# Kernel optimization log

Measured on AMD Instinct MI355X. Metric: run time of the kernel, lower is better.

The kernel has to match this reference:

```python
import jax, jax.numpy as jnp
import numpy as np

B, S, D = 4, 4096, 64
NEG = 1e31  # matches the torch module's -1e+31 masking constant


def setup_inputs() -> dict:
    key = jax.random.key(0)
    kq, kk, kv = jax.random.split(key, 3)
    return {
        "query": jax.random.normal(kq, (B, S, D), dtype=jnp.float32),
        "key": jax.random.normal(kk, (B, S, D), dtype=jnp.float32),
        "value": jax.random.normal(kv, (B, S, D), dtype=jnp.float32),
    }


def reference(query, key, value):
    # scores: [B, Sq, Sk]
    attn_weights = jnp.einsum("bqd,bkd->bqk", query, key)
    # NOTE: original subtracts the causal penalty BEFORE the sqrt(d) scaling
    Sq, Sk = query.shape[1], key.shape[1]
    causal_mask = jnp.triu(jnp.ones((Sq, Sk), dtype=attn_weights.dtype), k=1)
    attn_weights = attn_weights - causal_mask[None, :, :] * NEG
    attn_weights = attn_weights / np.sqrt(key.shape[-1]).astype(np.float32)
    attn_weights = jax.nn.softmax(attn_weights, axis=-1)
    # dropout p=0.0 -> identity on value
    attn_vec = jnp.einsum("bqk,bkd->bqd", attn_weights, value)
    return attn_vec, attn_weights
```

## Files before the change

### kernel.cpp

```cpp
#include <hip/hip_runtime.h>

#define SQ 4096
#define DD 64
#define NB 4
#define NEL (NB*SQ*DD)

typedef __attribute__((ext_vector_type(4))) float f32x4;
typedef __attribute__((ext_vector_type(8))) __bf16 bf16x8;

__device__ __forceinline__ unsigned short f2bf(float f) {
  unsigned int u = __builtin_bit_cast(unsigned int, f);
  u = (u + 0x7FFFu + ((u >> 16) & 1u)) >> 16;
  return (unsigned short)u;
}

__device__ __forceinline__ bf16x8 ldfrag(const unsigned short* p) {
  uint4 u = *(const uint4*)p;
  return __builtin_bit_cast(bf16x8, u);
}

__device__ __forceinline__ bf16x8 pack_bf8(f32x4 a, f32x4 b) {
  bf16x8 r;
  r[0] = (__bf16)a[0]; r[1] = (__bf16)a[1]; r[2] = (__bf16)a[2]; r[3] = (__bf16)a[3];
  r[4] = (__bf16)b[0]; r[5] = (__bf16)b[1]; r[6] = (__bf16)b[2]; r[7] = (__bf16)b[3];
  return r;
}

__global__ __launch_bounds__(256) void prep_kernel(
    const float* __restrict__ q, const float* __restrict__ k,
    const float* __restrict__ v, unsigned short* __restrict__ ws)
{
  unsigned short* qbf = ws;
  unsigned short* kbf = ws + (size_t)NEL;
  unsigned short* vt  = ws + 2*(size_t)NEL;
  const int bid = blockIdx.x;
  const int tid = threadIdx.x;
  if (bid < 1024) {
    const float* src = (bid < 512) ? q : k;
    unsigned short* dst = (bid < 512) ? qbf : kbf;
    const int base = (bid & 511) * 512 + tid;
#pragma unroll
    for (int i = 0; i < 2; ++i) {
      int idx = base + i * 256;
      float4 f = ((const float4*)src)[idx];
      ushort4 o;
      o.x = f2bf(f.x); o.y = f2bf(f.y); o.z = f2bf(f.z); o.w = f2bf(f.w);
      ((ushort4*)dst)[idx] = o;
    }
  } else {
    __shared__ unsigned short tile[64][66];
    const int t  = bid - 1024;
    const int bb = t >> 6;
    const int st = t & 63;
    const float* vb = v + (size_t)bb * SQ * DD + (size_t)st * 64 * DD;
    const int r  = tid >> 4;
    const int c4 = tid & 15;
#pragma unroll
    for (int j = 0; j < 4; ++j) {
      int row = r + j * 16;
      float4 f = ((const float4*)(vb + (size_t)row * DD))[c4];
      tile[row][c4 * 4 + 0] = f2bf(f.x);
      tile[row][c4 * 4 + 1] = f2bf(f.y);
      tile[row][c4 * 4 + 2] = f2bf(f.z);
      tile[row][c4 * 4 + 3] = f2bf(f.w);
    }
    __syncthreads();
    unsigned short* vtb = vt + (size_t)bb * DD * SQ;
#pragma unroll
    for (int j = 0; j < 4; ++j) {
      int d   = r + j * 16;
      int s0l = c4 * 4;
      ushort4 o;
      o.x = tile[s0l + 0][d];
      o.y = tile[s0l + 1][d];
      o.z = tile[s0l + 2][d];
      o.w = tile[s0l + 3][d];
      ((ushort4*)(vtb + (size_t)d * SQ + st * 64))[c4] = o;
    }
  }
}

__global__ __launch_bounds__(512, 6) void lsum_kernel(
    const unsigned short* __restrict__ qbf,
    const unsigned short* __restrict__ kbf,
    float* __restrict__ li2_g)
{
  __shared__ float lred[8][4][4];
  const int tid  = threadIdx.x;
  const int wave = tid >> 6;
  const int lane = tid & 63;
  const int l16  = lane & 15;
  const int quad = lane >> 4;

  const int bidx = blockIdx.x;
  const int b    = bidx & 3;
  const int qt   = 255 - (bidx >> 2);

  const unsigned short* Qb = qbf + (size_t)b * SQ * DD;
  const unsigned short* Kb = kbf + (size_t)b * SQ * DD;
  const int q0    = qt * 16;
  const int rowg0 = q0 + quad * 4;

  bf16x8 aQ0, aQ1;
  {
    const unsigned short* qrow = Qb + (size_t)(q0 + l16) * DD + quad * 8;
    aQ0 = ldfrag(qrow);
    aQ1 = ldfrag(qrow + 32);
  }

  const int nkt = (qt >> 2) + 1;
  const float SC = 0.125f * 1.4426950408889634f;
  const f32x4 zf = {0.f, 0.f, 0.f, 0.f};

  float lsum[4] = {0.f, 0.f, 0.f, 0.f};
  for (int kt = wave; kt < nkt; kt += 8) {
    const int k0 = kt * 64;
    f32x4 acc[4] = {zf, zf, zf, zf};
#pragma unroll
    for (int ct = 0; ct < 4; ++ct) {
      const unsigned short* krow = Kb + (size_t)(k0 + ct * 16 + l16) * DD + quad * 8;
      bf16x8 b0 = ldfrag(krow);
      bf16x8 b1 = ldfrag(krow + 32);
      acc[ct] = __builtin_amdgcn_mfma_f32_16x16x32_bf16(aQ0, b0, acc[ct], 0, 0, 0);
      acc[ct] = __builtin_amdgcn_mfma_f32_16x16x32_bf16(aQ1, b1, acc[ct], 0, 0, 0);
    }
#pragma unroll
    for (int ct = 0; ct < 4; ++ct) {
      const int colg = k0 + ct * 16 + l16;
#pragma unroll
      for (int r = 0; r < 4; ++r) {
        float tt = (colg <= rowg0 + r) ? acc[ct][r] * SC : -1e30f;
        lsum[r] += __builtin_amdgcn_exp2f(tt);
      }
    }
  }
#pragma unroll
  for (int r = 0; r < 4; ++r) {
    float v = lsum[r];
    v += __shfl_xor(v, 1);
    v += __shfl_xor(v, 2);
    v += __shfl_xor(v, 4);
    v += __shfl_xor(v, 8);
    lsum[r] = v;
  }
  if (l16 == 0) {
#pragma unroll
    for (int r = 0; r < 4; ++r) lred[wave][quad][r] = lsum[r];
  }
  __syncthreads();
  if (tid < 16) {
    float s = 0.f;
#pragma unroll
    for (int w = 0; w < 8; ++w) s += lred[w][tid >> 2][tid & 3];
    li2_g[(size_t)b * SQ + q0 + tid] = -__builtin_amdgcn_logf(s);
  }
}

__global__ __launch_bounds__(512, 4) void wo_kernel(
    const unsigned short* __restrict__ qbf,
    const unsigned short* __restrict__ kbf,
    const unsigned short* __restrict__ vtp,
    const float* __restrict__ li2_g,
    float* __restrict__ out_vec,
    float* __restrict__ out_w)
{
  __shared__ __align__(16) float pt[8][16][132];

  const int tid  = threadIdx.x;
  const int wave = tid >> 6;
  const int lane = tid & 63;
  const int l16  = lane & 15;
  const int quad = lane >> 4;
  const int half = lane >> 5;
  const int c32  = lane & 31;

  const int bidx = blockIdx.x;
  const int b    = bidx & 3;
  const int qt   = 255 - (bidx >> 2);

  const unsigned short* Qb = qbf + (size_t)b * SQ * DD;
  const unsigned short* Kb = kbf + (size_t)b * SQ * DD;
  const unsigned short* Vt = vtp + (size_t)b * DD * SQ;
  float* Wb = out_w  + (size_t)b * SQ * SQ;
  float* Ob = out_vec + (size_t)b * SQ * DD;

  const int q0    = qt * 16;
  const int rowg0 = q0 + quad * 4;

  bf16x8 aQ0, aQ1;
  {
    const unsigned short* qrow = Qb + (size_t)(q0 + l16) * DD + quad * 8;
    aQ0 = ldfrag(qrow);
    aQ1 = ldfrag(qrow + 32);
  }

  float li2[4];
#pragma unroll
  for (int r = 0; r < 4; ++r)
    li2[r] = li2_g[(size_t)b * SQ + rowg0 + r];

  const int nkt = (qt >> 2) + 1;
  const int nst = (nkt + 1) >> 1;
  const float SC = 0.125f * 1.4426950408889634f;
  const f32x4 zf = {0.f, 0.f, 0.f, 0.f};
  f32x4 accO[4] = {zf, zf, zf, zf};

  for (int st = wave; st < nst; st += 8) {
    const int k0c = st * 128;
#pragma unroll
    for (int h = 0; h < 2; ++h) {
      const int k0 = k0c + h * 64;
      f32x4 acc[4] = {zf, zf, zf, zf};
#pragma unroll
      for (int ct = 0; ct < 4; ++ct) {
        const unsigned short* krow = Kb + (size_t)(k0 + ct * 16 + l16) * DD + quad * 8;
        bf16x8 b0 = ldfrag(krow);
        bf16x8 b1 = ldfrag(krow + 32);
        acc[ct] = __builtin_amdgcn_mfma_f32_16x16x32_bf16(aQ0, b0, acc[ct], 0, 0, 0);
        acc[ct] = __builtin_amdgcn_mfma_f32_16x16x32_bf16(aQ1, b1, acc[ct], 0, 0, 0);
      }
#pragma unroll
      for (int ct = 0; ct < 4; ++ct) {
        const int colg = k0 + ct * 16 + l16;
#pragma unroll
        for (int r = 0; r < 4; ++r) {
          float tt = (colg <= rowg0 + r) ? __builtin_fmaf(acc[ct][r], SC, li2[r])
                                         : -1e30f;
          pt[wave][quad * 4 + r][h * 64 + ct * 16 + l16] = __builtin_amdgcn_exp2f(tt);
        }
      }
    }
#pragma unroll
    for (int i = 0; i < 8; ++i) {
      const int rr = 2 * i + half;
      f32x4 pv = *(const f32x4*)&pt[wave][rr][c32 * 4];
      *(f32x4*)(Wb + (size_t)(q0 + rr) * SQ + k0c + c32 * 4) = pv;
    }
#pragma unroll
    for (int kk = 0; kk < 4; ++kk) {
      const float* pr = &pt[wave][l16][kk * 32 + quad * 8];
      f32x4 p0 = *(const f32x4*)pr;
      f32x4 p1 = *(const f32x4*)(pr + 4);
      bf16x8 aP = pack_bf8(p0, p1);
#pragma unroll
      for (int ct = 0; ct < 4; ++ct) {
        const unsigned short* vrow =
            Vt + (size_t)(ct * 16 + l16) * SQ + k0c + kk * 32 + quad * 8;
        bf16x8 bv = ldfrag(vrow);
        accO[ct] = __builtin_amdgcn_mfma_f32_16x16x32_bf16(aP, bv, accO[ct], 0, 0, 0);
      }
    }
  }

  float* ow_mine = &pt[wave][0][0];
#pragma unroll
  for (int ct = 0; ct < 4; ++ct)
#pragma unroll
    for (int r = 0; r < 4; ++r)
      ow_mine[(quad * 4 + r) * 64 + ct * 16 + l16] = accO[ct][r];
  __syncthreads();
#pragma unroll
  for (int i = 0; i < 2; ++i) {
    int idx = tid + i * 512;
    int row = idx >> 6, col = idx & 63;
    float s = 0.f;
#pragma unroll
    for (int w = 0; w < 8; ++w) s += pt[w][0][row * 64 + col];
    Ob[(size_t)(q0 + row) * DD + col] = s;
  }

  const int zc0 = nst * 128;
  const int nz4 = (SQ - zc0) >> 2;
  if (nz4 > 0) {
    const f32x4 z = {0.f, 0.f, 0.f, 0.f};
    for (int r = 0; r < 16; ++r) {
      f32x4* zp = (f32x4*)(Wb + (size_t)(q0 + r) * SQ + zc0);
      for (int i = tid; i < nz4; i += 512)
        zp[i] = z;
    }
  }
}

extern "C" void kernel_launch(void* const* d_in, const int* in_sizes, int n_in,
                              void* d_out, int out_size, void* d_ws, size_t ws_size,
                              hipStream_t stream) {
  const float* q = (const float*)d_in[0];
  const float* k = (const float*)d_in[1];
  const float* v = (const float*)d_in[2];
  float* out_vec = (float*)d_out;
  float* out_w   = out_vec + (size_t)NB * SQ * DD;
  unsigned short* ws = (unsigned short*)d_ws;
  float* li2_g = (float*)(ws + 3 * (size_t)NEL);

  hipLaunchKernelGGL(prep_kernel, dim3(1280), dim3(256), 0, stream, q, k, v, ws);
  hipLaunchKernelGGL(lsum_kernel, dim3(1024), dim3(512), 0, stream,
                     ws, ws + (size_t)NEL, li2_g);
  hipLaunchKernelGGL(wo_kernel, dim3(1024), dim3(512), 0, stream,
                     ws, ws + (size_t)NEL, ws + 2 * (size_t)NEL,
                     li2_g, out_vec, out_w);
}
```

Before: 353.1 us.

## Stage 1024-column P strips in shared LDS for coalesced full-row weight stores

Each block now processes 1024-column super-strips in which every wave computes a 128-column slice into one shared LDS tile, then block-synchronises. Each wave writes two complete 1024-wide rows of the attention-weight matrix, so global stores become long contiguous row segments instead of 128-column fragments per wave. Slices above the diagonal are zero-filled in LDS rather than computed. This adds two __syncthreads per strip and can leave waves idle on partially live strips, which costs load balance in exchange for better write coalescing on the large weight output.

```diff
diff --git a/kernel.cpp b/kernel.cpp
--- a/kernel.cpp
+++ b/kernel.cpp
@@ -1,4 +1,5 @@
 #include <hip/hip_runtime.h>
+
 
 #define SQ 4096
 #define DD 64
@@ -164,15 +165,13 @@
     float* __restrict__ out_vec,
     float* __restrict__ out_w)
 {
-  __shared__ __align__(16) float pt[8][16][132];
+  __shared__ __align__(16) float ptS[16][1044];
 
   const int tid  = threadIdx.x;
-  const int wave = tid >> 6;
+  const int wv   = tid >> 6;
   const int lane = tid & 63;
   const int l16  = lane & 15;
   const int quad = lane >> 4;
-  const int half = lane >> 5;
-  const int c32  = lane & 31;
 
   const int bidx = blockIdx.x;
   const int b    = bidx & 3;
@@ -199,60 +198,88 @@
   for (int r = 0; r < 4; ++r)
     li2[r] = li2_g[(size_t)b * SQ + rowg0 + r];
 
-  const int nkt = (qt >> 2) + 1;
-  const int nst = (nkt + 1) >> 1;
+  const int nkt  = (qt >> 2) + 1;
+  const int ncov = nkt * 64;
+  const int nstb = (nkt + 15) >> 4;
   const float SC = 0.125f * 1.4426950408889634f;
   const f32x4 zf = {0.f, 0.f, 0.f, 0.f};
   f32x4 accO[4] = {zf, zf, zf, zf};
 
-  for (int st = wave; st < nst; st += 8) {
-    const int k0c = st * 128;
-#pragma unroll
-    for (int h = 0; h < 2; ++h) {
-      const int k0 = k0c + h * 64;
-      f32x4 acc[4] = {zf, zf, zf, zf};
-#pragma unroll
-      for (int ct = 0; ct < 4; ++ct) {
-        const unsigned short* krow = Kb + (size_t)(k0 + ct * 16 + l16) * DD + quad * 8;
-        bf16x8 b0 = ldfrag(krow);
-        bf16x8 b1 = ldfrag(krow + 32);
-        acc[ct] = __builtin_amdgcn_mfma_f32_16x16x32_bf16(aQ0, b0, acc[ct], 0, 0, 0);
-        acc[ct] = __builtin_amdgcn_mfma_f32_16x16x32_bf16(aQ1, b1, acc[ct], 0, 0, 0);
-      }
-#pragma unroll
-      for (int ct = 0; ct < 4; ++ct) {
-        const int colg = k0 + ct * 16 + l16;
-#pragma unroll
-        for (int r = 0; r < 4; ++r) {
-          float tt = (colg <= rowg0 + r) ? __builtin_fmaf(acc[ct][r], SC, li2[r])
-                                         : -1e30f;
-          pt[wave][quad * 4 + r][h * 64 + ct * 16 + l16] = __builtin_amdgcn_exp2f(tt);
+  const int wc0 = wv * 128;
+
+  for (int s = 0; s < nstb; ++s) {
+    const int k0s  = s << 10;
+    const int c0   = k0s + wc0;
+    const bool live = (c0 <= q0 + 15);
+
+    if (live) {
+#pragma unroll
+      for (int h = 0; h < 2; ++h) {
+        const int k0 = c0 + h * 64;
+        f32x4 acc[4] = {zf, zf, zf, zf};
+#pragma unroll
+        for (int ct = 0; ct < 4; ++ct) {
+          const unsigned short* krow = Kb + (size_t)(k0 + ct * 16 + l16) * DD + quad * 8;
+          bf16x8 b0 = ldfrag(krow);
+          bf16x8 b1 = ldfrag(krow + 32);
+          acc[ct] = __builtin_amdgcn_mfma_f32_16x16x32_bf16(aQ0, b0, acc[ct], 0, 0, 0);
+          acc[ct] = __builtin_amdgcn_mfma_f32_16x16x32_bf16(aQ1, b1, acc[ct], 0, 0, 0);
         }
-      }
-    }
-#pragma unroll
-    for (int i = 0; i < 8; ++i) {
-      const int rr = 2 * i + half;
-      f32x4 pv = *(const f32x4*)&pt[wave][rr][c32 * 4];
-      *(f32x4*)(Wb + (size_t)(q0 + rr) * SQ + k0c + c32 * 4) = pv;
-    }
-#pragma unroll
-    for (int kk = 0; kk < 4; ++kk) {
-      const float* pr = &pt[wave][l16][kk * 32 + quad * 8];
-      f32x4 p0 = *(const f32x4*)pr;
-      f32x4 p1 = *(const f32x4*)(pr + 4);
-      bf16x8 aP = pack_bf8(p0, p1);
-#pragma unroll
-      for (int ct = 0; ct < 4; ++ct) {
-        const unsigned short* vrow =
-            Vt + (size_t)(ct * 16 + l16) * SQ + k0c + kk * 32 + quad * 8;
-        bf16x8 bv = ldfrag(vrow);
-        accO[ct] = __builtin_amdgcn_mfma_f32_16x16x32_bf16(aP, bv, accO[ct], 0, 0, 0);
-      }
-    }
-  }
-
-  float* ow_mine = &pt[wave][0][0];
+#pragma unroll
+        for (int ct = 0; ct < 4; ++ct) {
+          const int colg = k0 + ct * 16 + l16;
+#pragma unroll
+          for (int r = 0; r < 4; ++r) {
+            float tt = (colg <= rowg0 + r) ? __builtin_fmaf(acc[ct][r], SC, li2[r])
+                                           : -1e30f;
+            ptS[quad * 4 + r][wc0 + h * 64 + ct * 16 + l16] =
+                __builtin_amdgcn_exp2f(tt);
+          }
+        }
+      }
+    } else {
+#pragma unroll
+      for (int i = 0; i < 8; ++i) {
+        int idx = i * 64 + lane;
+        int row = idx >> 5;
+        int c4  = idx & 31;
+        *(f32x4*)&ptS[row][wc0 + c4 * 4] = zf;
+      }
+    }
+    __syncthreads();
+
+#pragma unroll
+    for (int rr = 0; rr < 2; ++rr) {
+      const int row = 2 * wv + rr;
+      float* wrow = Wb + (size_t)(q0 + row) * SQ + k0s;
+#pragma unroll
+      for (int i = 0; i < 4; ++i) {
+        f32x4 pv = *(const f32x4*)&ptS[row][i * 256 + lane * 4];
+        *(f32x4*)(wrow + i * 256 + lane * 4) = pv;
+      }
+    }
+
+    if (live) {
+#pragma unroll
+      for (int kk = 0; kk < 4; ++kk) {
+        const float* pr = &ptS[l16][wc0 + kk * 32 + quad * 8];
+        f32x4 p0 = *(const f32x4*)pr;
+        f32x4 p1 = *(const f32x4*)(pr + 4);
+        bf16x8 aP = pack_bf8(p0, p1);
+#pragma unroll
+        for (int ct = 0; ct < 4; ++ct) {
+          const unsigned short* vrow =
+              Vt + (size_t)(ct * 16 + l16) * SQ + c0 + kk * 32 + quad * 8;
+          bf16x8 bv = ldfrag(vrow);
+          accO[ct] = __builtin_amdgcn_mfma_f32_16x16x32_bf16(aP, bv, accO[ct], 0, 0, 0);
+        }
+      }
+    }
+    __syncthreads();
+  }
+
+  float* base = &ptS[0][0];
+  float* ow_mine = base + wv * 2088;
 #pragma unroll
   for (int ct = 0; ct < 4; ++ct)
 #pragma unroll
@@ -265,18 +292,17 @@
     int row = idx >> 6, col = idx & 63;
     float s = 0.f;
 #pragma unroll
-    for (int w = 0; w < 8; ++w) s += pt[w][0][row * 64 + col];
+    for (int w = 0; w < 8; ++w) s += base[w * 2088 + row * 64 + col];
     Ob[(size_t)(q0 + row) * DD + col] = s;
   }
 
-  const int zc0 = nst * 128;
+  const int zc0 = nstb << 10;
   const int nz4 = (SQ - zc0) >> 2;
   if (nz4 > 0) {
-    const f32x4 z = {0.f, 0.f, 0.f, 0.f};
     for (int r = 0; r < 16; ++r) {
       f32x4* zp = (f32x4*)(Wb + (size_t)(q0 + r) * SQ + zc0);
       for (int i = tid; i < nz4; i += 512)
-        zp[i] = z;
+        zp[i] = zf;
     }
   }
 }
```

Result: no change. 348.4 us (-1.3%).

## Fuse row-sum and output passes into one kernel with LDS-resident probabilities

Applied to the files above, without the earlier changes.

Merges the separate softmax-denominator kernel and the weights/output kernel into one attention kernel. The unnormalized exp scores are computed once, stored as bf16 in a full-row LDS buffer (16 rows × 4104), and then normalized while being written out and fed to the PV MFMA. This drops the second QK^T recompute and a kernel launch. In exchange it uses about 131KB of LDS per block, which lowers occupancy to 2 blocks per CU. The stored weights are also now rounded to bf16 before normalization, which may cost accuracy.

```diff
diff --git a/kernel.cpp b/kernel.cpp
--- a/kernel.cpp
+++ b/kernel.cpp
@@ -1,9 +1,11 @@
 #include <hip/hip_runtime.h>
+
 
 #define SQ 4096
 #define DD 64
 #define NB 4
 #define NEL (NB*SQ*DD)
+#define PSTRIDE 4104
 
 typedef __attribute__((ext_vector_type(4))) float f32x4;
 typedef __attribute__((ext_vector_type(8))) __bf16 bf16x8;
@@ -19,11 +21,8 @@
   return __builtin_bit_cast(bf16x8, u);
 }
 
-__device__ __forceinline__ bf16x8 pack_bf8(f32x4 a, f32x4 b) {
-  bf16x8 r;
-  r[0] = (__bf16)a[0]; r[1] = (__bf16)a[1]; r[2] = (__bf16)a[2]; r[3] = (__bf16)a[3];
-  r[4] = (__bf16)b[0]; r[5] = (__bf16)b[1]; r[6] = (__bf16)b[2]; r[7] = (__bf16)b[3];
-  return r;
+__device__ __forceinline__ float bf2f(unsigned short u) {
+  return __builtin_bit_cast(float, (unsigned int)u << 16);
 }
 
 __global__ __launch_bounds__(256) void prep_kernel(
@@ -80,12 +79,17 @@
   }
 }
 
-__global__ __launch_bounds__(512, 6) void lsum_kernel(
+__global__ __launch_bounds__(512, 2) void attn_kernel(
     const unsigned short* __restrict__ qbf,
     const unsigned short* __restrict__ kbf,
-    float* __restrict__ li2_g)
+    const unsigned short* __restrict__ vtp,
+    float* __restrict__ out_vec,
+    float* __restrict__ out_w)
 {
+  __shared__ __align__(16) unsigned short Ps[16 * PSTRIDE];
   __shared__ float lred[8][4][4];
+  __shared__ float inv_l_s[16];
+
   const int tid  = threadIdx.x;
   const int wave = tid >> 6;
   const int lane = tid & 63;
@@ -98,6 +102,10 @@
 
   const unsigned short* Qb = qbf + (size_t)b * SQ * DD;
   const unsigned short* Kb = kbf + (size_t)b * SQ * DD;
+  const unsigned short* Vt = vtp + (size_t)b * DD * SQ;
+  float* Wb = out_w  + (size_t)b * SQ * SQ;
+  float* Ob = out_vec + (size_t)b * SQ * DD;
+
   const int q0    = qt * 16;
   const int rowg0 = q0 + quad * 4;
 
@@ -108,32 +116,52 @@
     aQ1 = ldfrag(qrow + 32);
   }
 
-  const int nkt = (qt >> 2) + 1;
+  const int nkt  = (qt >> 2) + 1;
+  const int nch  = (nkt + 15) >> 4;
+  const int nstp = nch << 3;
   const float SC = 0.125f * 1.4426950408889634f;
   const f32x4 zf = {0.f, 0.f, 0.f, 0.f};
 
   float lsum[4] = {0.f, 0.f, 0.f, 0.f};
-  for (int kt = wave; kt < nkt; kt += 8) {
-    const int k0 = kt * 64;
-    f32x4 acc[4] = {zf, zf, zf, zf};
-#pragma unroll
-    for (int ct = 0; ct < 4; ++ct) {
-      const unsigned short* krow = Kb + (size_t)(k0 + ct * 16 + l16) * DD + quad * 8;
-      bf16x8 b0 = ldfrag(krow);
-      bf16x8 b1 = ldfrag(krow + 32);
-      acc[ct] = __builtin_amdgcn_mfma_f32_16x16x32_bf16(aQ0, b0, acc[ct], 0, 0, 0);
-      acc[ct] = __builtin_amdgcn_mfma_f32_16x16x32_bf16(aQ1, b1, acc[ct], 0, 0, 0);
-    }
-#pragma unroll
-    for (int ct = 0; ct < 4; ++ct) {
-      const int colg = k0 + ct * 16 + l16;
-#pragma unroll
-      for (int r = 0; r < 4; ++r) {
-        float tt = (colg <= rowg0 + r) ? acc[ct][r] * SC : -1e30f;
-        lsum[r] += __builtin_amdgcn_exp2f(tt);
+  for (int st = wave; st < nstp; st += 8) {
+    const int k0c = st * 128;
+    if (k0c <= q0 + 15) {
+#pragma unroll
+      for (int h = 0; h < 2; ++h) {
+        const int k0 = k0c + h * 64;
+        f32x4 acc[4] = {zf, zf, zf, zf};
+#pragma unroll
+        for (int ct = 0; ct < 4; ++ct) {
+          const unsigned short* krow = Kb + (size_t)(k0 + ct * 16 + l16) * DD + quad * 8;
+          bf16x8 b0 = ldfrag(krow);
+          bf16x8 b1 = ldfrag(krow + 32);
+          acc[ct] = __builtin_amdgcn_mfma_f32_16x16x32_bf16(aQ0, b0, acc[ct], 0, 0, 0);
+          acc[ct] = __builtin_amdgcn_mfma_f32_16x16x32_bf16(aQ1, b1, acc[ct], 0, 0, 0);
+        }
+#pragma unroll
+        for (int ct = 0; ct < 4; ++ct) {
+          const int colg = k0 + ct * 16 + l16;
+#pragma unroll
+          for (int r = 0; r < 4; ++r) {
+            float tt = (colg <= rowg0 + r) ? acc[ct][r] * SC : -1e30f;
+            float p  = __builtin_amdgcn_exp2f(tt);
+            lsum[r] += p;
+            Ps[(quad * 4 + r) * PSTRIDE + colg] =
+                __builtin_bit_cast(unsigned short, (__bf16)p);
+          }
+        }
       }
-    }
-  }
+    } else {
+#pragma unroll
+      for (int h = 0; h < 2; ++h)
+#pragma unroll
+        for (int ct = 0; ct < 4; ++ct)
+#pragma unroll
+          for (int r = 0; r < 4; ++r)
+            Ps[(quad * 4 + r) * PSTRIDE + k0c + h * 64 + ct * 16 + l16] = 0;
+    }
+  }
+
 #pragma unroll
   for (int r = 0; r < 4; ++r) {
     float v = lsum[r];
@@ -152,112 +180,59 @@
     float s = 0.f;
 #pragma unroll
     for (int w = 0; w < 8; ++w) s += lred[w][tid >> 2][tid & 3];
-    li2_g[(size_t)b * SQ + q0 + tid] = -__builtin_amdgcn_logf(s);
-  }
-}
-
-__global__ __launch_bounds__(512, 4) void wo_kernel(
-    const unsigned short* __restrict__ qbf,
-    const unsigned short* __restrict__ kbf,
-    const unsigned short* __restrict__ vtp,
-    const float* __restrict__ li2_g,
-    float* __restrict__ out_vec,
-    float* __restrict__ out_w)
-{
-  __shared__ __align__(16) float pt[8][16][132];
-
-  const int tid  = threadIdx.x;
-  const int wave = tid >> 6;
-  const int lane = tid & 63;
-  const int l16  = lane & 15;
-  const int quad = lane >> 4;
-  const int half = lane >> 5;
-  const int c32  = lane & 31;
-
-  const int bidx = blockIdx.x;
-  const int b    = bidx & 3;
-  const int qt   = 255 - (bidx >> 2);
-
-  const unsigned short* Qb = qbf + (size_t)b * SQ * DD;
-  const unsigned short* Kb = kbf + (size_t)b * SQ * DD;
-  const unsigned short* Vt = vtp + (size_t)b * DD * SQ;
-  float* Wb = out_w  + (size_t)b * SQ * SQ;
-  float* Ob = out_vec + (size_t)b * SQ * DD;
-
-  const int q0    = qt * 16;
-  const int rowg0 = q0 + quad * 4;
-
-  bf16x8 aQ0, aQ1;
-  {
-    const unsigned short* qrow = Qb + (size_t)(q0 + l16) * DD + quad * 8;
-    aQ0 = ldfrag(qrow);
-    aQ1 = ldfrag(qrow + 32);
-  }
-
-  float li2[4];
-#pragma unroll
-  for (int r = 0; r < 4; ++r)
-    li2[r] = li2_g[(size_t)b * SQ + rowg0 + r];
-
-  const int nkt = (qt >> 2) + 1;
-  const int nst = (nkt + 1) >> 1;
-  const float SC = 0.125f * 1.4426950408889634f;
-  const f32x4 zf = {0.f, 0.f, 0.f, 0.f};
+    inv_l_s[tid] = 1.0f / s;
+  }
+  __syncthreads();
+
   f32x4 accO[4] = {zf, zf, zf, zf};
-
-  for (int st = wave; st < nst; st += 8) {
-    const int k0c = st * 128;
-#pragma unroll
-    for (int h = 0; h < 2; ++h) {
-      const int k0 = k0c + h * 64;
-      f32x4 acc[4] = {zf, zf, zf, zf};
-#pragma unroll
-      for (int ct = 0; ct < 4; ++ct) {
-        const unsigned short* krow = Kb + (size_t)(k0 + ct * 16 + l16) * DD + quad * 8;
-        bf16x8 b0 = ldfrag(krow);
-        bf16x8 b1 = ldfrag(krow + 32);
-        acc[ct] = __builtin_amdgcn_mfma_f32_16x16x32_bf16(aQ0, b0, acc[ct], 0, 0, 0);
-        acc[ct] = __builtin_amdgcn_mfma_f32_16x16x32_bf16(aQ1, b1, acc[ct], 0, 0, 0);
+  const int r0 = 2 * wave;
+
+  for (int ch = 0; ch < nch; ++ch) {
+    const int c0 = ch << 10;
+#pragma unroll
+    for (int rr = 0; rr < 2; ++rr) {
+      const int row = r0 + rr;
+      const float invr = inv_l_s[row];
+      const unsigned short* src = &Ps[row * PSTRIDE + c0];
+      float* dst = Wb + (size_t)(q0 + row) * SQ + c0;
+#pragma unroll
+      for (int g = 0; g < 4; ++g) {
+        ushort4 u = *(const ushort4*)(src + g * 256 + lane * 4);
+        f32x4 o;
+        o[0] = bf2f(u.x) * invr;
+        o[1] = bf2f(u.y) * invr;
+        o[2] = bf2f(u.z) * invr;
+        o[3] = bf2f(u.w) * invr;
+        *(f32x4*)(dst + g * 256 + lane * 4) = o;
       }
-#pragma unroll
-      for (int ct = 0; ct < 4; ++ct) {
-        const int colg = k0 + ct * 16 + l16;
-#pragma unroll
-        for (int r = 0; r < 4; ++r) {
-          float tt = (colg <= rowg0 + r) ? __builtin_fmaf(acc[ct][r], SC, li2[r])
-                                         : -1e30f;
-          pt[wave][quad * 4 + r][h * 64 + ct * 16 + l16] = __builtin_amdgcn_exp2f(tt);
+    }
+    const int sb = c0 + wave * 128;
+    if (sb <= q0 + 15) {
+#pragma unroll
+      for (int kk = 0; kk < 4; ++kk) {
+        const int cb = sb + kk * 32 + quad * 8;
+        bf16x8 aP = *(const bf16x8*)(&Ps[l16 * PSTRIDE + cb]);
+#pragma unroll
+        for (int ct = 0; ct < 4; ++ct) {
+          const unsigned short* vrow = Vt + (size_t)(ct * 16 + l16) * SQ + cb;
+          bf16x8 bv = ldfrag(vrow);
+          accO[ct] = __builtin_amdgcn_mfma_f32_16x16x32_bf16(aP, bv, accO[ct], 0, 0, 0);
         }
       }
     }
-#pragma unroll
-    for (int i = 0; i < 8; ++i) {
-      const int rr = 2 * i + half;
-      f32x4 pv = *(const f32x4*)&pt[wave][rr][c32 * 4];
-      *(f32x4*)(Wb + (size_t)(q0 + rr) * SQ + k0c + c32 * 4) = pv;
-    }
-#pragma unroll
-    for (int kk = 0; kk < 4; ++kk) {
-      const float* pr = &pt[wave][l16][kk * 32 + quad * 8];
-      f32x4 p0 = *(const f32x4*)pr;
-      f32x4 p1 = *(const f32x4*)(pr + 4);
-      bf16x8 aP = pack_bf8(p0, p1);
-#pragma unroll
-      for (int ct = 0; ct < 4; ++ct) {
-        const unsigned short* vrow =
-            Vt + (size_t)(ct * 16 + l16) * SQ + k0c + kk * 32 + quad * 8;
-        bf16x8 bv = ldfrag(vrow);
-        accO[ct] = __builtin_amdgcn_mfma_f32_16x16x32_bf16(aP, bv, accO[ct], 0, 0, 0);
-      }
-    }
-  }
-
-  float* ow_mine = &pt[wave][0][0];
+  }
+
+  float invq[4];
+#pragma unroll
+  for (int r = 0; r < 4; ++r) invq[r] = inv_l_s[quad * 4 + r];
+  __syncthreads();
+  float* stag = (float*)Ps;
+  float* ow = stag + wave * 1024;
 #pragma unroll
   for (int ct = 0; ct < 4; ++ct)
 #pragma unroll
     for (int r = 0; r < 4; ++r)
-      ow_mine[(quad * 4 + r) * 64 + ct * 16 + l16] = accO[ct][r];
+      ow[(quad * 4 + r) * 64 + ct * 16 + l16] = accO[ct][r] * invq[r];
   __syncthreads();
 #pragma unroll
   for (int i = 0; i < 2; ++i) {
@@ -265,18 +240,17 @@
     int row = idx >> 6, col = idx & 63;
     float s = 0.f;
 #pragma unroll
-    for (int w = 0; w < 8; ++w) s += pt[w][0][row * 64 + col];
+    for (int w = 0; w < 8; ++w) s += stag[w * 1024 + row * 64 + col];
     Ob[(size_t)(q0 + row) * DD + col] = s;
   }
 
-  const int zc0 = nst * 128;
+  const int zc0 = nch << 10;
   const int nz4 = (SQ - zc0) >> 2;
   if (nz4 > 0) {
-    const f32x4 z = {0.f, 0.f, 0.f, 0.f};
     for (int r = 0; r < 16; ++r) {
       f32x4* zp = (f32x4*)(Wb + (size_t)(q0 + r) * SQ + zc0);
       for (int i = tid; i < nz4; i += 512)
-        zp[i] = z;
+        zp[i] = zf;
     }
   }
 }
@@ -290,12 +264,9 @@
   float* out_vec = (float*)d_out;
   float* out_w   = out_vec + (size_t)NB * SQ * DD;
   unsigned short* ws = (unsigned short*)d_ws;
-  float* li2_g = (float*)(ws + 3 * (size_t)NEL);
 
   hipLaunchKernelGGL(prep_kernel, dim3(1280), dim3(256), 0, stream, q, k, v, ws);
-  hipLaunchKernelGGL(lsum_kernel, dim3(1024), dim3(512), 0, stream,
-                     ws, ws + (size_t)NEL, li2_g);
-  hipLaunchKernelGGL(wo_kernel, dim3(1024), dim3(512), 0, stream,
+  hipLaunchKernelGGL(attn_kernel, dim3(1024), dim3(512), 0, stream,
                      ws, ws + (size_t)NEL, ws + 2 * (size_t)NEL,
-                     li2_g, out_vec, out_w);
-}
+                     out_vec, out_w);
+}
```

Result: faster. 312.2 us (-11.6%).
